# Optimization experiments

Hardware: AMD Instinct MI355X
Metric: run time of the kernel (lower is better)

The kernel has to match this reference:

```python
import jax, jax.numpy as jnp
import numpy as np

N_HEAD = 16


def setup_inputs() -> dict:
    key = jax.random.key(0)
    k1, k2, k3 = jax.random.split(key, 3)
    B, T, C = 4, 2048, 1024
    x = jax.random.normal(k1, (B, T, C), dtype=jnp.float32)
    # Dense kernels (no bias), scaled like glorot-ish init
    W_attn = jax.random.normal(k2, (C, 3 * C), dtype=jnp.float32) * (1.0 / np.sqrt(C))
    W_proj = jax.random.normal(k3, (C, C), dtype=jnp.float32) * (1.0 / np.sqrt(C))
    return {"x": x, "W_attn": W_attn, "W_proj": W_proj}


def reference(x, W_attn, W_proj):
    # Vanilla causal multi-head self-attention (dropout is identity at inference).
    B, T, C = x.shape
    H = N_HEAD
    hs = C // H
    qkv = x @ W_attn                       # (B, T, 3C)
    q, k, v = jnp.split(qkv, 3, axis=-1)
    q = q.reshape(B, T, H, hs)             # (B, T, H, hs)
    k = k.reshape(B, T, H, hs)
    v = v.reshape(B, T, H, hs)
    scale = 1.0 / jnp.sqrt(jnp.asarray(hs, dtype=x.dtype))
    att = jnp.einsum('bthd,bshd->bhts', q, k) * scale   # (B, H, T, T)
    causal = jnp.tril(jnp.ones((T, T), dtype=bool))
    att = jnp.where(causal[None, None], att, -jnp.inf)
    att = jax.nn.softmax(att, axis=-1)
    y = jnp.einsum('bhts,bshd->bthd', att, v)            # (B, T, H, hs)
    y = y.reshape(B, T, C)
    return y @ W_proj
```

## Files before the change

### kernel.cpp

```cpp
#include <hip/hip_runtime.h>
#include <hip/hip_bf16.h>
#include <cstdint>
#include <cstddef>


typedef unsigned short ushort_t;
typedef __attribute__((ext_vector_type(8))) short short8;
typedef __attribute__((ext_vector_type(4))) float f32x4;
typedef __attribute__((ext_vector_type(16))) float f32x16;

#define AS1 __attribute__((address_space(1)))
#define AS3 __attribute__((address_space(3)))

#if __has_builtin(__builtin_amdgcn_exp2f)
#define EXP2(x) __builtin_amdgcn_exp2f(x)
#else
#define EXP2(x) exp2f(x)
#endif

__device__ __forceinline__ ushort_t f2bf(float f) {
  union { float f; unsigned u; } c; c.f = f;
  unsigned u = c.u;
  return (ushort_t)((u + 0x7FFFu + ((u >> 16) & 1u)) >> 16);
}

__device__ __forceinline__ unsigned cvt_pk_bf16(float a, float b) {
  unsigned r;
  asm("v_cvt_pk_bf16_f32 %0, %1, %2" : "=v"(r) : "v"(a), "v"(b));
  return r;
}

__global__ __launch_bounds__(256) void k_f32_to_bf16(const float* __restrict__ in,
                                                     ushort_t* __restrict__ out) {
  const size_t i = ((size_t)blockIdx.x * 256 + threadIdx.x) * 8;
  f32x4 a = *(const f32x4*)(in + i);
  f32x4 b = *(const f32x4*)(in + i + 4);
  short8 o;
  o[0] = (short)f2bf(a[0]); o[1] = (short)f2bf(a[1]);
  o[2] = (short)f2bf(a[2]); o[3] = (short)f2bf(a[3]);
  o[4] = (short)f2bf(b[0]); o[5] = (short)f2bf(b[1]);
  o[6] = (short)f2bf(b[2]); o[7] = (short)f2bf(b[3]);
  *(short8*)(out + i) = o;
}

__global__ __launch_bounds__(256) void k_transpose_bf16(const float* __restrict__ in,
                                                        ushort_t* __restrict__ out,
                                                        int R, int C) {
  __shared__ float tile[32][33];
  const int tx = threadIdx.x & 31, ty = threadIdx.x >> 5;
  const int c0 = blockIdx.x * 32, r0 = blockIdx.y * 32;
#pragma unroll
  for (int i = 0; i < 32; i += 8)
    tile[ty + i][tx] = in[(size_t)(r0 + ty + i) * C + c0 + tx];
  __syncthreads();
#pragma unroll
  for (int i = 0; i < 32; i += 8)
    out[(size_t)(c0 + ty + i) * R + r0 + tx] = f2bf(tile[tx][ty + i]);
}

__global__ __launch_bounds__(256) void k_vt(const ushort_t* __restrict__ qkv,
                                            ushort_t* __restrict__ vt) {
  __shared__ ushort_t tl[64][72];
  const int T = 2048, C3 = 3072;
  const int t0 = blockIdx.x * 64, h = blockIdx.y, b = blockIdx.z;
  const int r = threadIdx.x >> 4;
  const int c4 = (threadIdx.x & 15) * 4;
  const ushort_t* src = qkv + (size_t)(b * T + t0) * C3 + 2048 + h * 64;
#pragma unroll
  for (int p = 0; p < 4; p++) {
    const int row = p * 16 + r;
    *(short4*)&tl[row][c4] = *(const short4*)(src + (size_t)row * C3 + c4);
  }
  __syncthreads();
  ushort_t* dst = vt + (size_t)((b * 16 + h) * 64) * T + t0;
#pragma unroll
  for (int p = 0; p < 4; p++) {
    const int d = p * 16 + r;
    short4 o;
    o.x = (short)tl[c4 + 0][d];
    o.y = (short)tl[c4 + 1][d];
    o.z = (short)tl[c4 + 2][d];
    o.w = (short)tl[c4 + 3][d];
    *(short4*)(dst + (size_t)d * T + c4) = o;
  }
}

__device__ __forceinline__ void stage_unit(const ushort_t* __restrict__ X, int K,
                                           char* ldsbase, int tid, int w) {
#pragma unroll
  for (int j = 0; j < 2; j++) {
    const int rl = j * 64 + (tid >> 3);
    const int gc = ((tid & 7) ^ (rl & 7)) << 3;
    __builtin_amdgcn_global_load_lds(
        (const AS1 void*)(X + (size_t)rl * K + gc),
        (AS3 void*)(ldsbase + (j * 64 + w * 8) * 128), 16, 0, 0);
  }
}

template <int OUTMODE>
__global__ __launch_bounds__(512, 2) void k_gemm256(const ushort_t* __restrict__ A,
                                                    const ushort_t* __restrict__ Bt,
                                                    void* __restrict__ Cout,
                                                    ushort_t* __restrict__ vtout,
                                                    int N, int K) {
  __shared__ ushort_t As[3 * 256 * 64];
  __shared__ ushort_t Bs[3 * 128 * 64];

  const int tid = threadIdx.x;
  const int w = tid >> 6, lane = tid & 63;
  const int c = lane & 15, g = lane >> 4;
  const int wr = w >> 1, wc = w & 1;

  const int nwg = gridDim.x * gridDim.y;
  int wg = blockIdx.y * gridDim.x + blockIdx.x;
  {
    const int qd = nwg >> 3, rm = nwg & 7;
    const int xcd = wg & 7, idx = wg >> 3;
    wg = (xcd < rm ? xcd * (qd + 1) : rm * (qd + 1) + (xcd - rm) * qd) + idx;
  }
  const int bxn = wg % gridDim.x, by = wg / gridDim.x;

  const ushort_t* Abase = A + (size_t)(by * 256) * K;
  const ushort_t* Bbase = Bt + (size_t)(bxn * 128) * K;
  const int NT = K >> 6;

  auto stageT = [&](int tt) {
    const int s = tt % 3, k0 = tt * 64;
    char* Ab = (char*)As + s * 32768;
    char* Bb = (char*)Bs + s * 16384;
    stage_unit(Abase + k0, K, Ab, tid, w);
    stage_unit(Abase + (size_t)128 * K + k0, K, Ab + 16384, tid, w);
    stage_unit(Bbase + k0, K, Bb, tid, w);
  };

  f32x4 acc[4][4];
#pragma unroll
  for (int m = 0; m < 4; m++)
#pragma unroll
    for (int n = 0; n < 4; n++) acc[m][n] = (f32x4){0.f, 0.f, 0.f, 0.f};

  stageT(0);
  stageT(1);
  __builtin_amdgcn_sched_barrier(0);
  asm volatile("s_waitcnt vmcnt(6)" ::: "memory");
  __builtin_amdgcn_s_barrier();
  __builtin_amdgcn_sched_barrier(0);

  for (int t = 0; t < NT; ++t) {
    const int cur = t % 3;
    const char* Ab = (const char*)As + cur * 32768;
    const char* Bb = (const char*)Bs + cur * 16384;

    short8 af0[4], bv0[4], af1[4], bv1[4];
#pragma unroll
    for (int m = 0; m < 4; m++) {
      const int r = wr * 64 + m * 16 + c;
      const int sw = (r & 7) << 4;
      af0[m] = *(const short8*)(Ab + r * 128 + ((g * 16) ^ sw));
      af1[m] = *(const short8*)(Ab + r * 128 + ((64 + g * 16) ^ sw));
    }
#pragma unroll
    for (int n = 0; n < 4; n++) {
      const int r = wc * 64 + n * 16 + c;
      const int sw = (r & 7) << 4;
      bv0[n] = *(const short8*)(Bb + r * 128 + ((g * 16) ^ sw));
      bv1[n] = *(const short8*)(Bb + r * 128 + ((64 + g * 16) ^ sw));
    }
    if (t + 2 < NT) stageT(t + 2);

    __builtin_amdgcn_s_setprio(1);
#pragma unroll
    for (int m = 0; m < 4; m++)
#pragma unroll
      for (int n = 0; n < 4; n++)
        acc[m][n] = __builtin_amdgcn_mfma_f32_16x16x32_bf16(af0[m], bv0[n], acc[m][n], 0, 0, 0);
#pragma unroll
    for (int m = 0; m < 4; m++)
#pragma unroll
      for (int n = 0; n < 4; n++)
        acc[m][n] = __builtin_amdgcn_mfma_f32_16x16x32_bf16(af1[m], bv1[n], acc[m][n], 0, 0, 0);
    __builtin_amdgcn_s_setprio(0);

    if (t + 1 < NT) {
      __builtin_amdgcn_sched_barrier(0);
      if (t + 2 < NT)
        asm volatile("s_waitcnt vmcnt(6)" ::: "memory");
      else
        asm volatile("s_waitcnt vmcnt(0)" ::: "memory");
      __builtin_amdgcn_s_barrier();
      __builtin_amdgcn_sched_barrier(0);
    }
  }

  if (OUTMODE == 2 && bxn >= 16) {
#pragma unroll
    for (int m = 0; m < 4; m++)
#pragma unroll
      for (int n = 0; n < 4; n++) {
        const int cv = bxn * 128 + wc * 64 + n * 16 + c - 2048;
        const int hh = cv >> 6, d = cv & 63;
        const int row = by * 256 + wr * 64 + m * 16 + g * 4;
        const int bb = row >> 11, tt = row & 2047;
        short4 o;
        o.x = (short)f2bf(acc[m][n][0]);
        o.y = (short)f2bf(acc[m][n][1]);
        o.z = (short)f2bf(acc[m][n][2]);
        o.w = (short)f2bf(acc[m][n][3]);
        *(short4*)(vtout + ((size_t)((bb * 16 + hh) * 64 + d)) * 2048 + tt) = o;
      }
    return;
  }

#pragma unroll
  for (int m = 0; m < 4; m++)
#pragma unroll
    for (int n = 0; n < 4; n++) {
      const int col = bxn * 128 + wc * 64 + n * 16 + c;
#pragma unroll
      for (int r = 0; r < 4; r++) {
        const int row = by * 256 + wr * 64 + m * 16 + g * 4 + r;
        if (OUTMODE != 0)
          ((ushort_t*)Cout)[(size_t)row * N + col] = f2bf(acc[m][n][r]);
        else
          ((float*)Cout)[(size_t)row * N + col] = acc[m][n][r];
      }
    }
}

__device__ __forceinline__ void stage_kv(const ushort_t* __restrict__ Kp,
                                         const ushort_t* __restrict__ Vt,
                                         ushort_t* Kl, ushort_t* Vl,
                                         int kb, int wave, int lane) {
  const int C3 = 3072, T = 2048;
#pragma unroll
  for (int j = 0; j < 2; j++) {
    const int rbase = wave * 16 + j * 8;
    const int r = rbase + (lane >> 3);
    const int cbg = ((lane & 7) ^ (r & 7)) << 4;
    const int ldsbase = rbase * 128;
    __builtin_amdgcn_global_load_lds(
        (const AS1 void*)(Kp + (size_t)(kb + r) * C3 + (cbg >> 1)),
        (AS3 void*)((char*)Kl + ldsbase), 16, 0, 0);
    __builtin_amdgcn_global_load_lds(
        (const AS1 void*)(Vt + (size_t)r * T + kb + (cbg >> 1)),
        (AS3 void*)((char*)Vl + ldsbase), 16, 0, 0);
  }
}

__global__ __launch_bounds__(256, 2) void k_attn(const ushort_t* __restrict__ qkv,
                                                 const ushort_t* __restrict__ vt,
                                                 ushort_t* __restrict__ y) {
  const int T = 2048, C3 = 3072, Cc = 1024;
  __shared__ ushort_t Kl[2][64 * 64];
  __shared__ ushort_t Vl[2][64 * 64];

  const int tid = threadIdx.x;
  const int wave = tid >> 6, lane = tid & 63;
  const int l31 = lane & 31, hi = lane >> 5;
  const bool hib = (hi != 0);
  const int swr = (l31 & 7) << 4;
  const int b = blockIdx.z, h = blockIdx.y;
  const int tmap = ((int)blockIdx.x + ((b >> 1) << 3)) & 15;
  const int qi = (b & 1) ? (15 - tmap) : tmap;
  const int qbase = qi * 128 + wave * 32;
  const int q = qbase + l31;

  const size_t base = (size_t)b * T * C3 + h * 64;
  const ushort_t* Q = qkv + base;
  const ushort_t* Kp = qkv + base + 1024;
  const ushort_t* Vt = vt + (size_t)((b * 16 + h) * 64) * T;

  const float KS = 0.125f * 1.44269504f;
  const float THR = 8.0f;

  short8 qfr[4];
  {
    const ushort_t* qp = Q + (size_t)q * C3 + 8 * hi;
#pragma unroll
    for (int i = 0; i < 4; i++) qfr[i] = *(const short8*)(qp + 16 * i);
  }

  f32x16 yacc0 = (f32x16)(0.0f), yacc1 = (f32x16)(0.0f);
  float mx = -3.0e38f, ssum = 0.f;

  const int nk_blk = (qi + 1) * 128;
  stage_kv(Kp, Vt, Kl[0], Vl[0], 0, wave, lane);
  __syncthreads();
  int cur = 0;

  for (int kb = 0; kb < nk_blk; kb += 64) {
    if (kb + 64 < nk_blk)
      stage_kv(Kp, Vt, Kl[cur ^ 1], Vl[cur ^ 1], kb + 64, wave, lane);

    if (kb < qbase + 32) {
      const char* Kbuf = (const char*)Kl[cur];
      const char* Vbuf = (const char*)Vl[cur];

      f32x16 s0 = (f32x16)(0.0f), s1 = (f32x16)(0.0f);
#pragma unroll
      for (int i = 0; i < 4; i++) {
        const int colb = (32 * i + 16 * hi) ^ swr;
        const short8 ka0 = *(const short8*)(Kbuf + l31 * 128 + colb);
        const short8 ka1 = *(const short8*)(Kbuf + (32 + l31) * 128 + colb);
        s0 = __builtin_amdgcn_mfma_f32_32x32x16_bf16(ka0, qfr[i], s0, 0, 0, 0);
        s1 = __builtin_amdgcn_mfma_f32_32x32x16_bf16(ka1, qfr[i], s1, 0, 0, 0);
      }

      if (kb + 63 > qbase) {
#pragma unroll
        for (int r = 0; r < 16; r++) {
          const int key = kb + (r & 3) + 8 * (r >> 2) + 4 * hi;
          if (key > q) s0[r] = -1.0e30f;
          if (key + 32 > q) s1[r] = -1.0e30f;
        }
      }

      float t16[16];
#pragma unroll
      for (int r = 0; r < 16; r++) t16[r] = fmaxf(s0[r], s1[r]);
#pragma unroll
      for (int r = 0; r < 8; r++) t16[r] = fmaxf(t16[r], t16[r + 8]);
#pragma unroll
      for (int r = 0; r < 4; r++) t16[r] = fmaxf(t16[r], t16[r + 4]);
      float tm = fmaxf(fmaxf(t16[0], t16[1]), fmaxf(t16[2], t16[3]));
      tm = fmaxf(tm, __shfl_xor(tm, 32));
      const float cand = tm * KS;

      if (__any(cand > mx + THR)) {
        const float mnew = fmaxf(mx, cand);
        const float alpha = EXP2(mx - mnew);
        ssum *= alpha;
#pragma unroll
        for (int r = 0; r < 16; r++) { yacc0[r] *= alpha; yacc1[r] *= alpha; }
        mx = mnew;
      }

#pragma unroll
      for (int r = 0; r < 16; r++) {
        s0[r] = EXP2(__builtin_fmaf(s0[r], KS, -mx));
        s1[r] = EXP2(__builtin_fmaf(s1[r], KS, -mx));
      }
      {
        float ss[16];
#pragma unroll
        for (int r = 0; r < 16; r++) ss[r] = s0[r] + s1[r];
#pragma unroll
        for (int r = 0; r < 8; r++) ss[r] += ss[r + 8];
#pragma unroll
        for (int r = 0; r < 4; r++) ss[r] += ss[r + 4];
        float ts = (ss[0] + ss[1]) + (ss[2] + ss[3]);
        ts += __shfl_xor(ts, 32);
        ssum += ts;
      }

      union U4 { unsigned u[4]; short8 v; };
      U4 pb[4];
      {
        unsigned dw[4][4];
#pragma unroll
        for (int j = 0; j < 2; j++) {
          dw[j][0] = cvt_pk_bf16(s0[j * 8 + 0], s0[j * 8 + 1]);
          dw[j][1] = cvt_pk_bf16(s0[j * 8 + 2], s0[j * 8 + 3]);
          dw[j][2] = cvt_pk_bf16(s0[j * 8 + 4], s0[j * 8 + 5]);
          dw[j][3] = cvt_pk_bf16(s0[j * 8 + 6], s0[j * 8 + 7]);
          dw[2 + j][0] = cvt_pk_bf16(s1[j * 8 + 0], s1[j * 8 + 1]);
          dw[2 + j][1] = cvt_pk_bf16(s1[j * 8 + 2], s1[j * 8 + 3]);
          dw[2 + j][2] = cvt_pk_bf16(s1[j * 8 + 4], s1[j * 8 + 5]);
          dw[2 + j][3] = cvt_pk_bf16(s1[j * 8 + 6], s1[j * 8 + 7]);
        }
#pragma unroll
        for (int j = 0; j < 4; j++) {
          const unsigned d0 = dw[j][0], d1 = dw[j][1], d2 = dw[j][2], d3 = dw[j][3];
          const unsigned snd0 = hib ? d0 : d2;
          const unsigned snd1 = hib ? d1 : d3;
          const unsigned rcv0 = (unsigned)__shfl_xor((int)snd0, 32);
          const unsigned rcv1 = (unsigned)__shfl_xor((int)snd1, 32);
          pb[j].u[0] = hib ? rcv0 : d0;
          pb[j].u[1] = hib ? rcv1 : d1;
          pb[j].u[2] = hib ? d2 : rcv0;
          pb[j].u[3] = hib ? d3 : rcv1;
        }
      }

#pragma unroll
      for (int sj = 0; sj < 4; sj++) {
        const int colb = (sj * 32 + 16 * hi) ^ swr;
        const short8 va0 = *(const short8*)(Vbuf + l31 * 128 + colb);
        const short8 va1 = *(const short8*)(Vbuf + (32 + l31) * 128 + colb);
        yacc0 = __builtin_amdgcn_mfma_f32_32x32x16_bf16(va0, pb[sj].v, yacc0, 0, 0, 0);
        yacc1 = __builtin_amdgcn_mfma_f32_32x32x16_bf16(va1, pb[sj].v, yacc1, 0, 0, 0);
      }
    }

    __syncthreads();
    cur ^= 1;
  }

  const float inv = 1.0f / ssum;
  ushort_t* yp = y + (size_t)(b * T + q) * Cc + h * 64;
#pragma unroll
  for (int gi = 0; gi < 4; gi++) {
    short4 o0, o1;
    o0.x = (short)f2bf(yacc0[gi * 4 + 0] * inv);
    o0.y = (short)f2bf(yacc0[gi * 4 + 1] * inv);
    o0.z = (short)f2bf(yacc0[gi * 4 + 2] * inv);
    o0.w = (short)f2bf(yacc0[gi * 4 + 3] * inv);
    o1.x = (short)f2bf(yacc1[gi * 4 + 0] * inv);
    o1.y = (short)f2bf(yacc1[gi * 4 + 1] * inv);
    o1.z = (short)f2bf(yacc1[gi * 4 + 2] * inv);
    o1.w = (short)f2bf(yacc1[gi * 4 + 3] * inv);
    *(short4*)(yp + 8 * gi + 4 * hi) = o0;
    *(short4*)(yp + 32 + 8 * gi + 4 * hi) = o1;
  }
}

extern "C" void kernel_launch(void* const* d_in, const int* in_sizes, int n_in,
                              void* d_out, int out_size, void* d_ws, size_t ws_size,
                              hipStream_t stream) {
  const float* x = (const float*)d_in[0];
  const float* Wat = (const float*)d_in[1];
  const float* Wpr = (const float*)d_in[2];
  float* out = (float*)d_out;

  const int T = 2048, B = 4, H = 16, Cc = 1024;
  const int M = B * T;

  char* ws = (char*)d_ws;
  const size_t MB = 1024 * 1024;
  ushort_t* xb = (ushort_t*)ws;
  ushort_t* wat = (ushort_t*)(ws + 16 * MB);
  ushort_t* wpt = (ushort_t*)(ws + 24 * MB);
  ushort_t* qkv = (ushort_t*)(ws + 32 * MB);
  ushort_t* yb = (ushort_t*)(ws + 80 * MB);

  const bool big_ws = (ws_size >= (size_t)112 * MB);

  k_f32_to_bf16<<<dim3((M * Cc) / (8 * 256)), 256, 0, stream>>>(x, xb);
  k_transpose_bf16<<<dim3(3072 / 32, 1024 / 32), 256, 0, stream>>>(Wat, wat, 1024, 3072);
  k_transpose_bf16<<<dim3(1024 / 32, 1024 / 32), 256, 0, stream>>>(Wpr, wpt, 1024, 1024);

  if (big_ws) {
    ushort_t* vtb = (ushort_t*)(ws + 96 * MB);
    k_gemm256<2><<<dim3(3072 / 128, M / 256), 512, 0, stream>>>(xb, wat, qkv, vtb, 3072, 1024);
    k_attn<<<dim3(16, H, B), 256, 0, stream>>>(qkv, vtb, yb);
  } else {
    ushort_t* vtb = xb;
    k_gemm256<1><<<dim3(3072 / 128, M / 256), 512, 0, stream>>>(xb, wat, qkv, nullptr, 3072, 1024);
    k_vt<<<dim3(T / 64, H, B), 256, 0, stream>>>(qkv, vtb);
    k_attn<<<dim3(16, H, B), 256, 0, stream>>>(qkv, vtb, yb);
  }

  k_gemm256<0><<<dim3(1024 / 128, M / 256), 512, 0, stream>>>(yb, wpt, out, nullptr, 1024, 1024);
}
```

Baseline: 165.0 us.

## Split long causal query tiles across two blocks and merge partial softmax results

Query tiles in the second half of the sequence now have their key range split across two blocks. Each block writes an unnormalized bf16 partial output plus its row max and sum, and a new merge kernel combines them with log-sum-exp weighting. Work is balanced so every block handles at most 16 key tiles, which shortens the tail of the causal attention grid and raises the block count from 16 to 24 per head. The cost is an extra kernel launch, extra global traffic for the partials, and bf16 rounding of the partial outputs before the merge.

```diff
diff --git a/kernel.cpp b/kernel.cpp
--- a/kernel.cpp
+++ b/kernel.cpp
@@ -22,6 +22,11 @@
   union { float f; unsigned u; } c; c.f = f;
   unsigned u = c.u;
   return (ushort_t)((u + 0x7FFFu + ((u >> 16) & 1u)) >> 16);
+}
+
+__device__ __forceinline__ float bf2f(ushort_t u) {
+  union { unsigned u; float f; } c; c.u = ((unsigned)u) << 16;
+  return c.f;
 }
 
 __device__ __forceinline__ unsigned cvt_pk_bf16(float a, float b) {
@@ -247,9 +252,13 @@
   }
 }
 
+template <int SPLIT>
 __global__ __launch_bounds__(256, 2) void k_attn(const ushort_t* __restrict__ qkv,
                                                  const ushort_t* __restrict__ vt,
-                                                 ushort_t* __restrict__ y) {
+                                                 ushort_t* __restrict__ y,
+                                                 ushort_t* __restrict__ pA,
+                                                 ushort_t* __restrict__ pB,
+                                                 float* __restrict__ mls) {
   const int T = 2048, C3 = 3072, Cc = 1024;
   __shared__ ushort_t Kl[2][64 * 64];
   __shared__ ushort_t Vl[2][64 * 64];
@@ -260,10 +269,23 @@
   const bool hib = (hi != 0);
   const int swr = (l31 & 7) << 4;
   const int b = blockIdx.z, h = blockIdx.y;
-  const int tmap = ((int)blockIdx.x + ((b >> 1) << 3)) & 15;
-  const int qi = (b & 1) ? (15 - tmap) : tmap;
+
+  int qi, kt0, ktE, mode;
+  if (SPLIT) {
+    static const signed char TQI[24] = {8,9,10,11,12,13,14,15, 7,15, 6,14, 5,13, 4,12, 3,11, 2,10, 1,9, 0,8};
+    static const signed char TK0[24] = {0,0,0,0,0,0,0,0, 0,16, 0,16, 0,16, 0,16, 0,16, 0,16, 0,16, 0,16};
+    static const signed char TKE[24] = {16,16,16,16,16,16,16,16, 16,32, 14,30, 12,28, 10,26, 8,24, 6,22, 4,20, 2,18};
+    static const signed char TMD[24] = {1,1,1,1,1,1,1,1, 0,2, 0,2, 0,2, 0,2, 0,2, 0,2, 0,2, 0,2};
+    qi = TQI[blockIdx.x]; kt0 = TK0[blockIdx.x];
+    ktE = TKE[blockIdx.x]; mode = TMD[blockIdx.x];
+  } else {
+    const int tmap = ((int)blockIdx.x + ((b >> 1) << 3)) & 15;
+    qi = (b & 1) ? (15 - tmap) : tmap;
+    kt0 = 0; ktE = (qi + 1) * 2; mode = 0;
+  }
   const int qbase = qi * 128 + wave * 32;
   const int q = qbase + l31;
+  const int kbS = kt0 * 64, nk = ktE * 64;
 
   const size_t base = (size_t)b * T * C3 + h * 64;
   const ushort_t* Q = qkv + base;
@@ -283,13 +305,12 @@
   f32x16 yacc0 = (f32x16)(0.0f), yacc1 = (f32x16)(0.0f);
   float mx = -3.0e38f, ssum = 0.f;
 
-  const int nk_blk = (qi + 1) * 128;
-  stage_kv(Kp, Vt, Kl[0], Vl[0], 0, wave, lane);
+  stage_kv(Kp, Vt, Kl[0], Vl[0], kbS, wave, lane);
   __syncthreads();
   int cur = 0;
 
-  for (int kb = 0; kb < nk_blk; kb += 64) {
-    if (kb + 64 < nk_blk)
+  for (int kb = kbS; kb < nk; kb += 64) {
+    if (kb + 64 < nk)
       stage_kv(Kp, Vt, Kl[cur ^ 1], Vl[cur ^ 1], kb + 64, wave, lane);
 
     if (kb < qbase + 32) {
@@ -396,22 +417,71 @@
     cur ^= 1;
   }
 
-  const float inv = 1.0f / ssum;
-  ushort_t* yp = y + (size_t)(b * T + q) * Cc + h * 64;
-#pragma unroll
-  for (int gi = 0; gi < 4; gi++) {
-    short4 o0, o1;
-    o0.x = (short)f2bf(yacc0[gi * 4 + 0] * inv);
-    o0.y = (short)f2bf(yacc0[gi * 4 + 1] * inv);
-    o0.z = (short)f2bf(yacc0[gi * 4 + 2] * inv);
-    o0.w = (short)f2bf(yacc0[gi * 4 + 3] * inv);
-    o1.x = (short)f2bf(yacc1[gi * 4 + 0] * inv);
-    o1.y = (short)f2bf(yacc1[gi * 4 + 1] * inv);
-    o1.z = (short)f2bf(yacc1[gi * 4 + 2] * inv);
-    o1.w = (short)f2bf(yacc1[gi * 4 + 3] * inv);
-    *(short4*)(yp + 8 * gi + 4 * hi) = o0;
-    *(short4*)(yp + 32 + 8 * gi + 4 * hi) = o1;
-  }
+  if (mode == 0) {
+    const float inv = 1.0f / ssum;
+    ushort_t* yp = y + (size_t)(b * T + q) * Cc + h * 64;
+#pragma unroll
+    for (int gi = 0; gi < 4; gi++) {
+      short4 o0, o1;
+      o0.x = (short)f2bf(yacc0[gi * 4 + 0] * inv);
+      o0.y = (short)f2bf(yacc0[gi * 4 + 1] * inv);
+      o0.z = (short)f2bf(yacc0[gi * 4 + 2] * inv);
+      o0.w = (short)f2bf(yacc0[gi * 4 + 3] * inv);
+      o1.x = (short)f2bf(yacc1[gi * 4 + 0] * inv);
+      o1.y = (short)f2bf(yacc1[gi * 4 + 1] * inv);
+      o1.z = (short)f2bf(yacc1[gi * 4 + 2] * inv);
+      o1.w = (short)f2bf(yacc1[gi * 4 + 3] * inv);
+      *(short4*)(yp + 8 * gi + 4 * hi) = o0;
+      *(short4*)(yp + 32 + 8 * gi + 4 * hi) = o1;
+    }
+  } else {
+    const int pidx = (((b << 4) + h) << 10) + (q & 1023);
+    ushort_t* op = (mode == 1 ? pA : pB) + (size_t)pidx * 64;
+#pragma unroll
+    for (int gi = 0; gi < 4; gi++) {
+      short4 o0, o1;
+      o0.x = (short)f2bf(yacc0[gi * 4 + 0]);
+      o0.y = (short)f2bf(yacc0[gi * 4 + 1]);
+      o0.z = (short)f2bf(yacc0[gi * 4 + 2]);
+      o0.w = (short)f2bf(yacc0[gi * 4 + 3]);
+      o1.x = (short)f2bf(yacc1[gi * 4 + 0]);
+      o1.y = (short)f2bf(yacc1[gi * 4 + 1]);
+      o1.z = (short)f2bf(yacc1[gi * 4 + 2]);
+      o1.w = (short)f2bf(yacc1[gi * 4 + 3]);
+      *(short4*)(op + 8 * gi + 4 * hi) = o0;
+      *(short4*)(op + 32 + 8 * gi + 4 * hi) = o1;
+    }
+    if (hi == 0) {
+      float* mbuf = mls + (mode == 1 ? 0 : 131072);
+      mbuf[pidx] = mx;
+      mbuf[65536 + pidx] = ssum;
+    }
+  }
+}
+
+__global__ __launch_bounds__(256) void k_merge(const ushort_t* __restrict__ pA,
+                                               const ushort_t* __restrict__ pB,
+                                               const float* __restrict__ mls,
+                                               ushort_t* __restrict__ y) {
+  const int gtid = blockIdx.x * 256 + threadIdx.x;
+  const int row = gtid >> 4;
+  const int dq = (gtid & 15) << 2;
+  const int b = row >> 14, h = (row >> 10) & 15, qq = row & 1023;
+
+  const float ma = mls[row], la = mls[65536 + row];
+  const float mb = mls[131072 + row], lb = mls[196608 + row];
+  const float m = fmaxf(ma, mb);
+  const float wa = EXP2(ma - m), wb = EXP2(mb - m);
+  const float inv = 1.0f / (wa * la + wb * lb);
+
+  const short4 oa = *(const short4*)(pA + (size_t)row * 64 + dq);
+  const short4 ob = *(const short4*)(pB + (size_t)row * 64 + dq);
+  short4 o;
+  o.x = (short)f2bf((wa * bf2f((ushort_t)oa.x) + wb * bf2f((ushort_t)ob.x)) * inv);
+  o.y = (short)f2bf((wa * bf2f((ushort_t)oa.y) + wb * bf2f((ushort_t)ob.y)) * inv);
+  o.z = (short)f2bf((wa * bf2f((ushort_t)oa.z) + wb * bf2f((ushort_t)ob.z)) * inv);
+  o.w = (short)f2bf((wa * bf2f((ushort_t)oa.w) + wb * bf2f((ushort_t)ob.w)) * inv);
+  *(short4*)(y + ((size_t)(b * 2048 + 1024 + qq) * 1024) + h * 64 + dq) = o;
 }
 
 extern "C" void kernel_launch(void* const* d_in, const int* in_sizes, int n_in,
@@ -429,9 +499,12 @@
   const size_t MB = 1024 * 1024;
   ushort_t* xb = (ushort_t*)ws;
   ushort_t* wat = (ushort_t*)(ws + 16 * MB);
+  float* mls = (float*)(ws + 22 * MB);
   ushort_t* wpt = (ushort_t*)(ws + 24 * MB);
   ushort_t* qkv = (ushort_t*)(ws + 32 * MB);
   ushort_t* yb = (ushort_t*)(ws + 80 * MB);
+  ushort_t* pA = (ushort_t*)ws;
+  ushort_t* pB = (ushort_t*)(ws + 8 * MB);
 
   const bool big_ws = (ws_size >= (size_t)112 * MB);
 
@@ -442,12 +515,13 @@
   if (big_ws) {
     ushort_t* vtb = (ushort_t*)(ws + 96 * MB);
     k_gemm256<2><<<dim3(3072 / 128, M / 256), 512, 0, stream>>>(xb, wat, qkv, vtb, 3072, 1024);
-    k_attn<<<dim3(16, H, B), 256, 0, stream>>>(qkv, vtb, yb);
+    k_attn<1><<<dim3(24, H, B), 256, 0, stream>>>(qkv, vtb, yb, pA, pB, mls);
+    k_merge<<<dim3(65536 * 16 / 256), 256, 0, stream>>>(pA, pB, mls, yb);
   } else {
     ushort_t* vtb = xb;
     k_gemm256<1><<<dim3(3072 / 128, M / 256), 512, 0, stream>>>(xb, wat, qkv, nullptr, 3072, 1024);
     k_vt<<<dim3(T / 64, H, B), 256, 0, stream>>>(qkv, vtb);
-    k_attn<<<dim3(16, H, B), 256, 0, stream>>>(qkv, vtb, yb);
+    k_attn<0><<<dim3(16, H, B), 256, 0, stream>>>(qkv, vtb, yb, nullptr, nullptr, nullptr);
   }
 
   k_gemm256<0><<<dim3(1024 / 128, M / 256), 512, 0, stream>>>(yb, wpt, out, nullptr, 1024, 1024);
```

Result: slower. 176.6 us (+7.0%).

## Pair light and heavy causal query tiles per block sharing staged K/V

Applied to the files above, without the earlier changes.

Each attention block now handles two query tiles, A and 15-A, so every block does the same amount of causal work. The two tiles share one pass of K/V staging through LDS, which halves the K/V load traffic for the shorter tile, and the grid shrinks from 16 to 8 blocks along x. The cost is doubled register state per wave (two Q fragment sets, two output accumulators, two score sets), which may cut occupancy under launch_bounds(256,2) or cause spills. There are also half as many blocks to fill the GPU.

```diff
diff --git a/kernel.cpp b/kernel.cpp
--- a/kernel.cpp
+++ b/kernel.cpp
@@ -227,6 +227,109 @@
     }
 }
 
+union U4 { unsigned u[4]; short8 v; };
+
+__device__ __forceinline__ void sm_pack(f32x16& s0, f32x16& s1, float& mx,
+                                        float& ssum, f32x16& y0, f32x16& y1,
+                                        U4 (&pb)[4], int q, int qbase, int kb,
+                                        bool hib, int hi) {
+  const float KS = 0.125f * 1.44269504f;
+  const float THR = 8.0f;
+
+  if (kb + 63 > qbase) {
+#pragma unroll
+    for (int r = 0; r < 16; r++) {
+      const int key = kb + (r & 3) + 8 * (r >> 2) + 4 * hi;
+      if (key > q) s0[r] = -1.0e30f;
+      if (key + 32 > q) s1[r] = -1.0e30f;
+    }
+  }
+
+  float t16[16];
+#pragma unroll
+  for (int r = 0; r < 16; r++) t16[r] = fmaxf(s0[r], s1[r]);
+#pragma unroll
+  for (int r = 0; r < 8; r++) t16[r] = fmaxf(t16[r], t16[r + 8]);
+#pragma unroll
+  for (int r = 0; r < 4; r++) t16[r] = fmaxf(t16[r], t16[r + 4]);
+  float tm = fmaxf(fmaxf(t16[0], t16[1]), fmaxf(t16[2], t16[3]));
+  tm = fmaxf(tm, __shfl_xor(tm, 32));
+  const float cand = tm * KS;
+
+  if (__any(cand > mx + THR)) {
+    const float mnew = fmaxf(mx, cand);
+    const float alpha = EXP2(mx - mnew);
+    ssum *= alpha;
+#pragma unroll
+    for (int r = 0; r < 16; r++) { y0[r] *= alpha; y1[r] *= alpha; }
+    mx = mnew;
+  }
+
+#pragma unroll
+  for (int r = 0; r < 16; r++) {
+    s0[r] = EXP2(__builtin_fmaf(s0[r], KS, -mx));
+    s1[r] = EXP2(__builtin_fmaf(s1[r], KS, -mx));
+  }
+  {
+    float ss[16];
+#pragma unroll
+    for (int r = 0; r < 16; r++) ss[r] = s0[r] + s1[r];
+#pragma unroll
+    for (int r = 0; r < 8; r++) ss[r] += ss[r + 8];
+#pragma unroll
+    for (int r = 0; r < 4; r++) ss[r] += ss[r + 4];
+    float ts = (ss[0] + ss[1]) + (ss[2] + ss[3]);
+    ts += __shfl_xor(ts, 32);
+    ssum += ts;
+  }
+
+  unsigned dw[4][4];
+#pragma unroll
+  for (int j = 0; j < 2; j++) {
+    dw[j][0] = cvt_pk_bf16(s0[j * 8 + 0], s0[j * 8 + 1]);
+    dw[j][1] = cvt_pk_bf16(s0[j * 8 + 2], s0[j * 8 + 3]);
+    dw[j][2] = cvt_pk_bf16(s0[j * 8 + 4], s0[j * 8 + 5]);
+    dw[j][3] = cvt_pk_bf16(s0[j * 8 + 6], s0[j * 8 + 7]);
+    dw[2 + j][0] = cvt_pk_bf16(s1[j * 8 + 0], s1[j * 8 + 1]);
+    dw[2 + j][1] = cvt_pk_bf16(s1[j * 8 + 2], s1[j * 8 + 3]);
+    dw[2 + j][2] = cvt_pk_bf16(s1[j * 8 + 4], s1[j * 8 + 5]);
+    dw[2 + j][3] = cvt_pk_bf16(s1[j * 8 + 6], s1[j * 8 + 7]);
+  }
+#pragma unroll
+  for (int j = 0; j < 4; j++) {
+    const unsigned d0 = dw[j][0], d1 = dw[j][1], d2 = dw[j][2], d3 = dw[j][3];
+    const unsigned snd0 = hib ? d0 : d2;
+    const unsigned snd1 = hib ? d1 : d3;
+    const unsigned rcv0 = (unsigned)__shfl_xor((int)snd0, 32);
+    const unsigned rcv1 = (unsigned)__shfl_xor((int)snd1, 32);
+    pb[j].u[0] = hib ? rcv0 : d0;
+    pb[j].u[1] = hib ? rcv1 : d1;
+    pb[j].u[2] = hib ? d2 : rcv0;
+    pb[j].u[3] = hib ? d3 : rcv1;
+  }
+}
+
+__device__ __forceinline__ void store_frag(ushort_t* __restrict__ y, int b, int q,
+                                           int h, int hi, const f32x16& y0,
+                                           const f32x16& y1, float ssum) {
+  const float inv = 1.0f / ssum;
+  ushort_t* yp = y + (size_t)(b * 2048 + q) * 1024 + h * 64;
+#pragma unroll
+  for (int gi = 0; gi < 4; gi++) {
+    short4 o0, o1;
+    o0.x = (short)f2bf(y0[gi * 4 + 0] * inv);
+    o0.y = (short)f2bf(y0[gi * 4 + 1] * inv);
+    o0.z = (short)f2bf(y0[gi * 4 + 2] * inv);
+    o0.w = (short)f2bf(y0[gi * 4 + 3] * inv);
+    o1.x = (short)f2bf(y1[gi * 4 + 0] * inv);
+    o1.y = (short)f2bf(y1[gi * 4 + 1] * inv);
+    o1.z = (short)f2bf(y1[gi * 4 + 2] * inv);
+    o1.w = (short)f2bf(y1[gi * 4 + 3] * inv);
+    *(short4*)(yp + 8 * gi + 4 * hi) = o0;
+    *(short4*)(yp + 32 + 8 * gi + 4 * hi) = o1;
+  }
+}
+
 __device__ __forceinline__ void stage_kv(const ushort_t* __restrict__ Kp,
                                          const ushort_t* __restrict__ Vt,
                                          ushort_t* Kl, ushort_t* Vl,
@@ -250,7 +353,7 @@
 __global__ __launch_bounds__(256, 2) void k_attn(const ushort_t* __restrict__ qkv,
                                                  const ushort_t* __restrict__ vt,
                                                  ushort_t* __restrict__ y) {
-  const int T = 2048, C3 = 3072, Cc = 1024;
+  const int T = 2048, C3 = 3072;
   __shared__ ushort_t Kl[2][64 * 64];
   __shared__ ushort_t Vl[2][64 * 64];
 
@@ -260,135 +363,75 @@
   const bool hib = (hi != 0);
   const int swr = (l31 & 7) << 4;
   const int b = blockIdx.z, h = blockIdx.y;
-  const int tmap = ((int)blockIdx.x + ((b >> 1) << 3)) & 15;
-  const int qi = (b & 1) ? (15 - tmap) : tmap;
-  const int qbase = qi * 128 + wave * 32;
-  const int q = qbase + l31;
+  const int A = (b & 2) ? (7 - (int)blockIdx.x) : (int)blockIdx.x;
+  const int qbA = A * 128 + wave * 32;
+  const int qbB = (15 - A) * 128 + wave * 32;
+  const int qA = qbA + l31, qB = qbB + l31;
 
   const size_t base = (size_t)b * T * C3 + h * 64;
   const ushort_t* Q = qkv + base;
   const ushort_t* Kp = qkv + base + 1024;
   const ushort_t* Vt = vt + (size_t)((b * 16 + h) * 64) * T;
 
-  const float KS = 0.125f * 1.44269504f;
-  const float THR = 8.0f;
-
-  short8 qfr[4];
+  short8 qfrA[4], qfrB[4];
   {
-    const ushort_t* qp = Q + (size_t)q * C3 + 8 * hi;
-#pragma unroll
-    for (int i = 0; i < 4; i++) qfr[i] = *(const short8*)(qp + 16 * i);
-  }
-
-  f32x16 yacc0 = (f32x16)(0.0f), yacc1 = (f32x16)(0.0f);
-  float mx = -3.0e38f, ssum = 0.f;
-
-  const int nk_blk = (qi + 1) * 128;
+    const ushort_t* qpA = Q + (size_t)qA * C3 + 8 * hi;
+    const ushort_t* qpB = Q + (size_t)qB * C3 + 8 * hi;
+#pragma unroll
+    for (int i = 0; i < 4; i++) {
+      qfrA[i] = *(const short8*)(qpA + 16 * i);
+      qfrB[i] = *(const short8*)(qpB + 16 * i);
+    }
+  }
+
+  f32x16 yA0 = (f32x16)(0.0f), yA1 = (f32x16)(0.0f);
+  f32x16 yB0 = (f32x16)(0.0f), yB1 = (f32x16)(0.0f);
+  float mxA = -3.0e38f, ssA = 0.f, mxB = -3.0e38f, ssB = 0.f;
+
+  const int nk = (16 - A) * 128;
   stage_kv(Kp, Vt, Kl[0], Vl[0], 0, wave, lane);
   __syncthreads();
   int cur = 0;
 
-  for (int kb = 0; kb < nk_blk; kb += 64) {
-    if (kb + 64 < nk_blk)
+  for (int kb = 0; kb < nk; kb += 64) {
+    if (kb + 64 < nk)
       stage_kv(Kp, Vt, Kl[cur ^ 1], Vl[cur ^ 1], kb + 64, wave, lane);
 
-    if (kb < qbase + 32) {
+    if (kb < qbB + 32) {
+      const bool liveA = kb < qbA + 32;
       const char* Kbuf = (const char*)Kl[cur];
       const char* Vbuf = (const char*)Vl[cur];
 
-      f32x16 s0 = (f32x16)(0.0f), s1 = (f32x16)(0.0f);
+      f32x16 sA0 = (f32x16)(0.0f), sA1 = (f32x16)(0.0f);
+      f32x16 sB0 = (f32x16)(0.0f), sB1 = (f32x16)(0.0f);
 #pragma unroll
       for (int i = 0; i < 4; i++) {
         const int colb = (32 * i + 16 * hi) ^ swr;
         const short8 ka0 = *(const short8*)(Kbuf + l31 * 128 + colb);
         const short8 ka1 = *(const short8*)(Kbuf + (32 + l31) * 128 + colb);
-        s0 = __builtin_amdgcn_mfma_f32_32x32x16_bf16(ka0, qfr[i], s0, 0, 0, 0);
-        s1 = __builtin_amdgcn_mfma_f32_32x32x16_bf16(ka1, qfr[i], s1, 0, 0, 0);
-      }
-
-      if (kb + 63 > qbase) {
-#pragma unroll
-        for (int r = 0; r < 16; r++) {
-          const int key = kb + (r & 3) + 8 * (r >> 2) + 4 * hi;
-          if (key > q) s0[r] = -1.0e30f;
-          if (key + 32 > q) s1[r] = -1.0e30f;
+        sB0 = __builtin_amdgcn_mfma_f32_32x32x16_bf16(ka0, qfrB[i], sB0, 0, 0, 0);
+        sB1 = __builtin_amdgcn_mfma_f32_32x32x16_bf16(ka1, qfrB[i], sB1, 0, 0, 0);
+        if (liveA) {
+          sA0 = __builtin_amdgcn_mfma_f32_32x32x16_bf16(ka0, qfrA[i], sA0, 0, 0, 0);
+          sA1 = __builtin_amdgcn_mfma_f32_32x32x16_bf16(ka1, qfrA[i], sA1, 0, 0, 0);
         }
       }
 
-      float t16[16];
-#pragma unroll
-      for (int r = 0; r < 16; r++) t16[r] = fmaxf(s0[r], s1[r]);
-#pragma unroll
-      for (int r = 0; r < 8; r++) t16[r] = fmaxf(t16[r], t16[r + 8]);
-#pragma unroll
-      for (int r = 0; r < 4; r++) t16[r] = fmaxf(t16[r], t16[r + 4]);
-      float tm = fmaxf(fmaxf(t16[0], t16[1]), fmaxf(t16[2], t16[3]));
-      tm = fmaxf(tm, __shfl_xor(tm, 32));
-      const float cand = tm * KS;
-
-      if (__any(cand > mx + THR)) {
-        const float mnew = fmaxf(mx, cand);
-        const float alpha = EXP2(mx - mnew);
-        ssum *= alpha;
-#pragma unroll
-        for (int r = 0; r < 16; r++) { yacc0[r] *= alpha; yacc1[r] *= alpha; }
-        mx = mnew;
-      }
-
-#pragma unroll
-      for (int r = 0; r < 16; r++) {
-        s0[r] = EXP2(__builtin_fmaf(s0[r], KS, -mx));
-        s1[r] = EXP2(__builtin_fmaf(s1[r], KS, -mx));
-      }
-      {
-        float ss[16];
-#pragma unroll
-        for (int r = 0; r < 16; r++) ss[r] = s0[r] + s1[r];
-#pragma unroll
-        for (int r = 0; r < 8; r++) ss[r] += ss[r + 8];
-#pragma unroll
-        for (int r = 0; r < 4; r++) ss[r] += ss[r + 4];
-        float ts = (ss[0] + ss[1]) + (ss[2] + ss[3]);
-        ts += __shfl_xor(ts, 32);
-        ssum += ts;
-      }
-
-      union U4 { unsigned u[4]; short8 v; };
-      U4 pb[4];
-      {
-        unsigned dw[4][4];
-#pragma unroll
-        for (int j = 0; j < 2; j++) {
-          dw[j][0] = cvt_pk_bf16(s0[j * 8 + 0], s0[j * 8 + 1]);
-          dw[j][1] = cvt_pk_bf16(s0[j * 8 + 2], s0[j * 8 + 3]);
-          dw[j][2] = cvt_pk_bf16(s0[j * 8 + 4], s0[j * 8 + 5]);
-          dw[j][3] = cvt_pk_bf16(s0[j * 8 + 6], s0[j * 8 + 7]);
-          dw[2 + j][0] = cvt_pk_bf16(s1[j * 8 + 0], s1[j * 8 + 1]);
-          dw[2 + j][1] = cvt_pk_bf16(s1[j * 8 + 2], s1[j * 8 + 3]);
-          dw[2 + j][2] = cvt_pk_bf16(s1[j * 8 + 4], s1[j * 8 + 5]);
-          dw[2 + j][3] = cvt_pk_bf16(s1[j * 8 + 6], s1[j * 8 + 7]);
-        }
-#pragma unroll
-        for (int j = 0; j < 4; j++) {
-          const unsigned d0 = dw[j][0], d1 = dw[j][1], d2 = dw[j][2], d3 = dw[j][3];
-          const unsigned snd0 = hib ? d0 : d2;
-          const unsigned snd1 = hib ? d1 : d3;
-          const unsigned rcv0 = (unsigned)__shfl_xor((int)snd0, 32);
-          const unsigned rcv1 = (unsigned)__shfl_xor((int)snd1, 32);
-          pb[j].u[0] = hib ? rcv0 : d0;
-          pb[j].u[1] = hib ? rcv1 : d1;
-          pb[j].u[2] = hib ? d2 : rcv0;
-          pb[j].u[3] = hib ? d3 : rcv1;
-        }
-      }
+      U4 pbA[4], pbB[4];
+      sm_pack(sB0, sB1, mxB, ssB, yB0, yB1, pbB, qB, qbB, kb, hib, hi);
+      if (liveA) sm_pack(sA0, sA1, mxA, ssA, yA0, yA1, pbA, qA, qbA, kb, hib, hi);
 
 #pragma unroll
       for (int sj = 0; sj < 4; sj++) {
         const int colb = (sj * 32 + 16 * hi) ^ swr;
         const short8 va0 = *(const short8*)(Vbuf + l31 * 128 + colb);
         const short8 va1 = *(const short8*)(Vbuf + (32 + l31) * 128 + colb);
-        yacc0 = __builtin_amdgcn_mfma_f32_32x32x16_bf16(va0, pb[sj].v, yacc0, 0, 0, 0);
-        yacc1 = __builtin_amdgcn_mfma_f32_32x32x16_bf16(va1, pb[sj].v, yacc1, 0, 0, 0);
+        yB0 = __builtin_amdgcn_mfma_f32_32x32x16_bf16(va0, pbB[sj].v, yB0, 0, 0, 0);
+        yB1 = __builtin_amdgcn_mfma_f32_32x32x16_bf16(va1, pbB[sj].v, yB1, 0, 0, 0);
+        if (liveA) {
+          yA0 = __builtin_amdgcn_mfma_f32_32x32x16_bf16(va0, pbA[sj].v, yA0, 0, 0, 0);
+          yA1 = __builtin_amdgcn_mfma_f32_32x32x16_bf16(va1, pbA[sj].v, yA1, 0, 0, 0);
+        }
       }
     }
 
@@ -396,22 +439,8 @@
     cur ^= 1;
   }
 
-  const float inv = 1.0f / ssum;
-  ushort_t* yp = y + (size_t)(b * T + q) * Cc + h * 64;
-#pragma unroll
-  for (int gi = 0; gi < 4; gi++) {
-    short4 o0, o1;
-    o0.x = (short)f2bf(yacc0[gi * 4 + 0] * inv);
-    o0.y = (short)f2bf(yacc0[gi * 4 + 1] * inv);
-    o0.z = (short)f2bf(yacc0[gi * 4 + 2] * inv);
-    o0.w = (short)f2bf(yacc0[gi * 4 + 3] * inv);
-    o1.x = (short)f2bf(yacc1[gi * 4 + 0] * inv);
-    o1.y = (short)f2bf(yacc1[gi * 4 + 1] * inv);
-    o1.z = (short)f2bf(yacc1[gi * 4 + 2] * inv);
-    o1.w = (short)f2bf(yacc1[gi * 4 + 3] * inv);
-    *(short4*)(yp + 8 * gi + 4 * hi) = o0;
-    *(short4*)(yp + 32 + 8 * gi + 4 * hi) = o1;
-  }
+  store_frag(y, b, qA, h, hi, yA0, yA1, ssA);
+  store_frag(y, b, qB, h, hi, yB0, yB1, ssB);
 }
 
 extern "C" void kernel_launch(void* const* d_in, const int* in_sizes, int n_in,
@@ -442,12 +471,12 @@
   if (big_ws) {
     ushort_t* vtb = (ushort_t*)(ws + 96 * MB);
     k_gemm256<2><<<dim3(3072 / 128, M / 256), 512, 0, stream>>>(xb, wat, qkv, vtb, 3072, 1024);
-    k_attn<<<dim3(16, H, B), 256, 0, stream>>>(qkv, vtb, yb);
+    k_attn<<<dim3(8, H, B), 256, 0, stream>>>(qkv, vtb, yb);
   } else {
     ushort_t* vtb = xb;
     k_gemm256<1><<<dim3(3072 / 128, M / 256), 512, 0, stream>>>(xb, wat, qkv, nullptr, 3072, 1024);
     k_vt<<<dim3(T / 64, H, B), 256, 0, stream>>>(qkv, vtb);
-    k_attn<<<dim3(16, H, B), 256, 0, stream>>>(qkv, vtb, yb);
+    k_attn<<<dim3(8, H, B), 256, 0, stream>>>(qkv, vtb, yb);
   }
 
   k_gemm256<0><<<dim3(1024 / 128, M / 256), 512, 0, stream>>>(yb, wpt, out, nullptr, 1024, 1024);
```

Result: slower. 170.5 us (+3.3%).
